# Optimization experiments

Hardware: AMD Instinct MI355X
Metric: run time of the kernel (lower is better)

The kernel has to match this reference:

```python
import jax, jax.numpy as jnp
import numpy as np
import math

D_MODEL = 1024
N_HEADS = 16
B, T = 4, 2048


def setup_inputs() -> dict:
    key = jax.random.key(0)
    ks = jax.random.split(key, 10)
    s = 1.0 / math.sqrt(D_MODEL)
    x = jax.random.normal(ks[0], (B, T, D_MODEL), dtype=jnp.float32)
    # causal mask, broadcastable over batch and heads; 0 -> masked
    mask = jnp.tril(jnp.ones((T, T), dtype=jnp.int32))[None, None, :, :]
    w_q = jax.random.normal(ks[1], (D_MODEL, D_MODEL), dtype=jnp.float32) * s
    b_q = jnp.zeros((D_MODEL,), dtype=jnp.float32)
    w_k = jax.random.normal(ks[2], (D_MODEL, D_MODEL), dtype=jnp.float32) * s
    b_k = jnp.zeros((D_MODEL,), dtype=jnp.float32)
    w_v = jax.random.normal(ks[3], (D_MODEL, D_MODEL), dtype=jnp.float32) * s
    b_v = jnp.zeros((D_MODEL,), dtype=jnp.float32)
    w_o = jax.random.normal(ks[4], (D_MODEL, D_MODEL), dtype=jnp.float32) * s
    b_o = jnp.zeros((D_MODEL,), dtype=jnp.float32)
    return {"x": x, "mask": mask, "w_q": w_q, "b_q": b_q, "w_k": w_k,
            "b_k": b_k, "w_v": w_v, "b_v": b_v, "w_o": w_o, "b_o": b_o}


def reference(x, mask, w_q, b_q, w_k, b_k, w_v, b_v, w_o, b_o):
    Bx, Tx, C = x.shape
    H = N_HEADS
    d_k = C // H
    def split_heads(y):  # [B,T,C] -> [B,H,T,d_k]
        return y.reshape(Bx, Tx, H, d_k).transpose(0, 2, 1, 3)
    Q = split_heads(x @ w_q + b_q)
    K = split_heads(x @ w_k + b_k)
    V = split_heads(x @ w_v + b_v)
    scores = jnp.einsum('bhqd,bhkd->bhqk', Q, K) / math.sqrt(d_k)
    scores = jnp.where(mask == 0, jnp.float32(-1e9), scores)
    attn = jax.nn.softmax(scores, axis=-1)
    out = jnp.einsum('bhqk,bhkd->bhqd', attn, V)
    out = out.transpose(0, 2, 1, 3).reshape(Bx, Tx, C)
    return out @ w_o + b_o
```

## Files before the change

### kernel.cpp

```cpp
#include <hip/hip_runtime.h>
#include <stdint.h>

#define D_MODEL 1024
#define NH      16
#define BB      4
#define TT      2048
#define MROWS   (BB * TT)

typedef __attribute__((ext_vector_type(8))) short bf16x8;
typedef __attribute__((ext_vector_type(4))) float f32x4;

__device__ __forceinline__ unsigned short f2bf(float f) {
    union { float f; unsigned int u; } v; v.f = f;
    unsigned int r = v.u + 0x7fffu + ((v.u >> 16) & 1u);
    return (unsigned short)(r >> 16);
}

__device__ __forceinline__ unsigned short f2bf_fast(float f) {
    union { float f; unsigned int u; } v; v.f = f;
    return (unsigned short)((v.u + 0x8000u) >> 16);
}

__device__ __forceinline__ void gload_lds16(const unsigned short* g, unsigned short* l) {
    __builtin_amdgcn_global_load_lds(
        (const __attribute__((address_space(1))) void*)g,
        (__attribute__((address_space(3))) void*)l,
        16, 0, 0);
}

__global__ void convert_x_kernel(const float* __restrict__ x, unsigned short* __restrict__ xb) {
    int i = blockIdx.x * 256 + threadIdx.x;
    float4 v = ((const float4*)x)[i];
    ushort4 o;
    o.x = f2bf(v.x); o.y = f2bf(v.y); o.z = f2bf(v.z); o.w = f2bf(v.w);
    ((ushort4*)xb)[i] = o;
}

__global__ void transpose_w_kernel(const float* __restrict__ wq, const float* __restrict__ wk,
                                   const float* __restrict__ wv, const float* __restrict__ wo,
                                   unsigned short* tq, unsigned short* tk,
                                   unsigned short* tv, unsigned short* to_) {
    const float* src; unsigned short* dst;
    switch (blockIdx.z) {
        case 0:  src = wq; dst = tq; break;
        case 1:  src = wk; dst = tk; break;
        case 2:  src = wv; dst = tv; break;
        default: src = wo; dst = to_; break;
    }
    __shared__ float tile[32][33];
    int tx = threadIdx.x & 31, ty = threadIdx.x >> 5;
    int k0 = blockIdx.y * 32, n0 = blockIdx.x * 32;
    #pragma unroll
    for (int i = 0; i < 4; ++i)
        tile[ty + i * 8][tx] = src[(k0 + ty + i * 8) * D_MODEL + n0 + tx];
    __syncthreads();
    #pragma unroll
    for (int i = 0; i < 4; ++i)
        dst[(n0 + ty + i * 8) * D_MODEL + k0 + tx] = f2bf(tile[tx][ty + i * 8]);
}

__device__ __forceinline__ void gemm_mainloop(const unsigned short* __restrict__ A,
                                              const unsigned short* __restrict__ Bt,
                                              int m0, int n0,
                                              unsigned short* As, unsigned short* Bs,
                                              f32x4 acc[4][4]) {
    const int tid = threadIdx.x;
    const int lane = tid & 63, wave = tid >> 6;
    const int wm = (wave >> 1) * 64, wn = (wave & 1) * 64;
    const int l15 = lane & 15, quad = lane >> 4;
    const int rx7 = l15 & 7;
    const int srow = tid >> 3;
    const int scol = ((tid & 7) ^ (srow & 7)) * 8;
    const unsigned short* Ag = A + (size_t)(m0 + srow) * D_MODEL + scol;
    const unsigned short* Bg = Bt + (size_t)(n0 + srow) * D_MODEL + scol;
    unsigned short* AsW = As + wave * 512;
    unsigned short* BsW = Bs + wave * 512;
    for (int k0 = 0; k0 < D_MODEL; k0 += 64) {
        __syncthreads();
        #pragma unroll
        for (int p = 0; p < 4; ++p) {
            gload_lds16(Ag + k0 + (size_t)(32 * p) * D_MODEL, AsW + (32 * p) * 64);
            gload_lds16(Bg + k0 + (size_t)(32 * p) * D_MODEL, BsW + (32 * p) * 64);
        }
        __syncthreads();
        #pragma unroll
        for (int kk = 0; kk < 2; ++kk) {
            const int co = ((kk * 4 + quad) ^ rx7) * 8;
            bf16x8 af[4], bfr[4];
            #pragma unroll
            for (int mt = 0; mt < 4; ++mt)
                af[mt] = *(const bf16x8*)(As + (wm + mt * 16 + l15) * 64 + co);
            #pragma unroll
            for (int nt = 0; nt < 4; ++nt)
                bfr[nt] = *(const bf16x8*)(Bs + (wn + nt * 16 + l15) * 64 + co);
            #pragma unroll
            for (int mt = 0; mt < 4; ++mt)
                #pragma unroll
                for (int nt = 0; nt < 4; ++nt)
                    acc[mt][nt] = __builtin_amdgcn_mfma_f32_16x16x32_bf16(af[mt], bfr[nt], acc[mt][nt], 0, 0, 0);
        }
    }
}

__global__ __launch_bounds__(256, 2) void gemm_qkv_kernel(
        const unsigned short* __restrict__ Xb, const unsigned short* __restrict__ Wt,
        const float* __restrict__ bq, const float* __restrict__ bk, const float* __restrict__ bv,
        unsigned short* __restrict__ Qo, unsigned short* __restrict__ Ko,
        unsigned short* __restrict__ VTo) {
    __shared__ unsigned short S[18432];
    unsigned short* As = S;
    unsigned short* Bs = S + 8192;
    int m0 = blockIdx.y * 128, n0 = blockIdx.x * 128;
    f32x4 acc[4][4];
    #pragma unroll
    for (int mt = 0; mt < 4; ++mt)
        #pragma unroll
        for (int nt = 0; nt < 4; ++nt)
            acc[mt][nt] = (f32x4){0.f, 0.f, 0.f, 0.f};
    gemm_mainloop(Xb, Wt, m0, n0, As, Bs, acc);

    const int sel = n0 >> 10;
    const float* bias = (sel == 0) ? bq : (sel == 1) ? bk : bv;
    const float scale = (sel == 0) ? 0.125f * 1.44269504f : 1.f;
    const int tid = threadIdx.x, lane = tid & 63, wave = tid >> 6;
    const int wm = (wave >> 1) * 64, wn = (wave & 1) * 64, l15 = lane & 15, quad = lane >> 4;
    if (sel < 2) {
        unsigned short* Out = (sel == 0) ? Qo : Ko;
        __syncthreads();
        unsigned short* R = S + (wn >> 6) * 9216;
        #pragma unroll
        for (int nt = 0; nt < 4; ++nt) {
            int ln = nt * 16 + l15;
            int col = (n0 + wn + nt * 16 + l15) & 1023;
            float bv_ = bias[col];
            #pragma unroll
            for (int mt = 0; mt < 4; ++mt)
                #pragma unroll
                for (int r = 0; r < 4; ++r) {
                    int lm = wm + mt * 16 + quad * 4 + r;
                    R[lm * 72 + ln] = f2bf((acc[mt][nt][r] + bv_) * scale);
                }
        }
        __syncthreads();
        int hh = tid >> 7, t = tid & 127;
        int h0 = (n0 & 1023) >> 6;
        int b = m0 >> 11, tb = m0 & 2047;
        unsigned short* gp = Out + (size_t)((b * NH + h0 + hh) * TT + tb + t) * 64;
        const unsigned short* lp = S + hh * 9216 + t * 72;
        #pragma unroll
        for (int j = 0; j < 8; ++j)
            *(uint4*)(gp + j * 8) = *(const uint4*)(lp + j * 8);
    } else {
        #pragma unroll
        for (int nt = 0; nt < 4; ++nt) {
            int col = (n0 + wn + nt * 16 + l15) & 1023;
            float bv_ = bias[col];
            int h = col >> 6, dd = col & 63;
            #pragma unroll
            for (int mt = 0; mt < 4; ++mt) {
                int gm0 = m0 + wm + mt * 16 + quad * 4;
                int b = gm0 >> 11, t0 = gm0 & 2047;
                ushort4 o;
                o.x = f2bf(acc[mt][nt][0] + bv_);
                o.y = f2bf(acc[mt][nt][1] + bv_);
                o.z = f2bf(acc[mt][nt][2] + bv_);
                o.w = f2bf(acc[mt][nt][3] + bv_);
                *(ushort4*)&VTo[(((size_t)(b * NH + h) * 16 + (t0 >> 7)) * 64 + dd) * 128 + (t0 & 127)] = o;
            }
        }
    }
}

__global__ __launch_bounds__(256, 2) void gemm_out_kernel(
        const unsigned short* __restrict__ Ob, const unsigned short* __restrict__ Wto,
        const float* __restrict__ bo, float* __restrict__ out) {
    __shared__ unsigned short As[128 * 64], Bs[128 * 64];
    int m0 = blockIdx.y * 128, n0 = blockIdx.x * 128;
    f32x4 acc[4][4];
    #pragma unroll
    for (int mt = 0; mt < 4; ++mt)
        #pragma unroll
        for (int nt = 0; nt < 4; ++nt)
            acc[mt][nt] = (f32x4){0.f, 0.f, 0.f, 0.f};
    gemm_mainloop(Ob, Wto, m0, n0, As, Bs, acc);
    const int tid = threadIdx.x, lane = tid & 63, wave = tid >> 6;
    const int wm = (wave >> 1) * 64, wn = (wave & 1) * 64, l15 = lane & 15, quad = lane >> 4;
    #pragma unroll
    for (int nt = 0; nt < 4; ++nt) {
        int gn = n0 + wn + nt * 16 + l15;
        float bv_ = bo[gn];
        #pragma unroll
        for (int mt = 0; mt < 4; ++mt) {
            #pragma unroll
            for (int r = 0; r < 4; ++r) {
                int gm = m0 + wm + mt * 16 + quad * 4 + r;
                out[(size_t)gm * D_MODEL + gn] = acc[mt][nt][r] + bv_;
            }
        }
    }
}

__global__ __launch_bounds__(256, 2) void flash_kernel(
        const unsigned short* __restrict__ Q, const unsigned short* __restrict__ K,
        const unsigned short* __restrict__ VT, unsigned short* __restrict__ O) {
    __shared__ unsigned short Kd[2][8192];
    __shared__ unsigned short Vd[2][8192];
    __shared__ unsigned short Ps[5120];
    const int n = blockIdx.x;
    const int bh = n & 63;
    const int qt = 15 - (n >> 6);
    const int q0 = qt * 128;
    const int tid = threadIdx.x, lane = tid & 63, wave = tid >> 6;
    const int l15 = lane & 15, quad = lane >> 4;
    const int mbase = wave * 32;
    const unsigned short* Qb = Q + (size_t)bh * (TT * 64) + (size_t)q0 * 64;
    const unsigned short* Kb = K + (size_t)bh * (TT * 64);
    const unsigned short* Vtb = VT + (size_t)bh * (16 * 8192);
    unsigned short* Pw = Ps + wave * 1280;

    int koff[4], voff[4];
    #pragma unroll
    for (int p = 0; p < 4; ++p) {
        int c = p * 256 + wave * 64 + lane;
        int kr = c >> 3, ks = c & 7;
        koff[p] = kr * 64 + ((ks ^ (kr & 7)) * 8);
        int vd = c >> 4, vs = c & 15;
        voff[p] = vd * 128 + ((vs ^ (vd & 15)) * 8);
    }
    auto fire = [&](int kt, int buf) {
        const unsigned short* Ksrc = Kb + kt * 8192;
        const unsigned short* Vsrc = Vtb + kt * 8192;
        #pragma unroll
        for (int p = 0; p < 4; ++p) {
            gload_lds16(Ksrc + koff[p], &Kd[buf][(p * 256 + wave * 64) * 8]);
            gload_lds16(Vsrc + voff[p], &Vd[buf][(p * 256 + wave * 64) * 8]);
        }
    };

    bf16x8 qf[2][2];
    #pragma unroll
    for (int mt = 0; mt < 2; ++mt)
        #pragma unroll
        for (int kk = 0; kk < 2; ++kk)
            qf[mt][kk] = *(const bf16x8*)(Qb + (size_t)(mbase + mt * 16 + l15) * 64 + kk * 32 + quad * 8);

    float l_part[2][4];
    f32x4 acc[2][4];
    #pragma unroll
    for (int mt = 0; mt < 2; ++mt) {
        #pragma unroll
        for (int r = 0; r < 4; ++r) l_part[mt][r] = 0.f;
        #pragma unroll
        for (int nt = 0; nt < 4; ++nt) acc[mt][nt] = (f32x4){0.f, 0.f, 0.f, 0.f};
    }

    fire(0, 0);

    for (int kt = 0; kt <= qt; ++kt) {
        const int p = kt & 1;
        __syncthreads();
        if (kt < qt) fire(kt + 1, p ^ 1);
        const unsigned short* Ksl = Kd[p];
        const unsigned short* Vsl = Vd[p];

        #pragma unroll 1
        for (int s4 = 0; s4 < 4; ++s4) {
            f32x4 sf[2][2];
            #pragma unroll
            for (int mt = 0; mt < 2; ++mt)
                #pragma unroll
                for (int ntl = 0; ntl < 2; ++ntl) sf[mt][ntl] = (f32x4){0.f, 0.f, 0.f, 0.f};
            #pragma unroll
            for (int kk = 0; kk < 2; ++kk)
                #pragma unroll
                for (int ntl = 0; ntl < 2; ++ntl) {
                    int row = s4 * 32 + ntl * 16 + l15;
                    bf16x8 kf = *(const bf16x8*)&Ksl[row * 64 + (((kk * 4 + quad) ^ (row & 7)) * 8)];
                    #pragma unroll
                    for (int mt = 0; mt < 2; ++mt)
                        sf[mt][ntl] = __builtin_amdgcn_mfma_f32_16x16x32_bf16(qf[mt][kk], kf, sf[mt][ntl], 0, 0, 0);
                }
            if (kt == qt) {
                #pragma unroll
                for (int mt = 0; mt < 2; ++mt)
                    #pragma unroll
                    for (int ntl = 0; ntl < 2; ++ntl)
                        #pragma unroll
                        for (int r = 0; r < 4; ++r) {
                            int qi = mbase + mt * 16 + quad * 4 + r;
                            int ki = s4 * 32 + ntl * 16 + l15;
                            if (ki > qi) sf[mt][ntl][r] = -1e30f;
                        }
            }
            #pragma unroll
            for (int mt = 0; mt < 2; ++mt)
                #pragma unroll
                for (int ntl = 0; ntl < 2; ++ntl)
                    #pragma unroll
                    for (int r = 0; r < 4; ++r) {
                        float pv = __builtin_amdgcn_exp2f(sf[mt][ntl][r]);
                        l_part[mt][r] += pv;
                        Pw[(mt * 16 + quad * 4 + r) * 40 + ntl * 16 + l15] = f2bf_fast(pv);
                    }
            bf16x8 pa[2];
            #pragma unroll
            for (int mt = 0; mt < 2; ++mt)
                pa[mt] = *(const bf16x8*)&Pw[(mt * 16 + l15) * 40 + quad * 8];
            #pragma unroll
            for (int ntv = 0; ntv < 4; ++ntv) {
                int d = ntv * 16 + l15;
                bf16x8 vf = *(const bf16x8*)&Vsl[d * 128 + (((s4 * 4 + quad) ^ (d & 15)) * 8)];
                #pragma unroll
                for (int mt = 0; mt < 2; ++mt)
                    acc[mt][ntv] = __builtin_amdgcn_mfma_f32_16x16x32_bf16(pa[mt], vf, acc[mt][ntv], 0, 0, 0);
            }
        }
    }

    const int b = bh >> 4, h = bh & 15;
    float inv[2][4];
    #pragma unroll
    for (int mt = 0; mt < 2; ++mt)
        #pragma unroll
        for (int r = 0; r < 4; ++r) {
            float l = l_part[mt][r];
            l += __shfl_xor(l, 1); l += __shfl_xor(l, 2);
            l += __shfl_xor(l, 4); l += __shfl_xor(l, 8);
            inv[mt][r] = __builtin_amdgcn_rcpf(l);
        }
    __syncthreads();
    unsigned short* Ost = &Kd[0][0];
    #pragma unroll
    for (int mt = 0; mt < 2; ++mt)
        #pragma unroll
        for (int nt = 0; nt < 4; ++nt)
            #pragma unroll
            for (int r = 0; r < 4; ++r)
                Ost[(mbase + mt * 16 + quad * 4 + r) * 72 + nt * 16 + l15] =
                    f2bf(acc[mt][nt][r] * inv[mt][r]);
    __syncthreads();
    {
        int row = tid >> 1, seg = tid & 1;
        unsigned short* gp = O + (size_t)(b * TT + q0 + row) * D_MODEL + h * 64 + seg * 32;
        const unsigned short* lp = Ost + row * 72 + seg * 32;
        #pragma unroll
        for (int j = 0; j < 4; ++j)
            *(uint4*)(gp + j * 8) = *(const uint4*)(lp + j * 8);
    }
}

extern "C" void kernel_launch(void* const* d_in, const int* in_sizes, int n_in,
                              void* d_out, int out_size, void* d_ws, size_t ws_size,
                              hipStream_t stream) {
    const float* x  = (const float*)d_in[0];
    const float* wq = (const float*)d_in[2];
    const float* bq = (const float*)d_in[3];
    const float* wk = (const float*)d_in[4];
    const float* bk = (const float*)d_in[5];
    const float* wv = (const float*)d_in[6];
    const float* bv = (const float*)d_in[7];
    const float* wo = (const float*)d_in[8];
    const float* bo = (const float*)d_in[9];

    char* ws = (char*)d_ws;
    unsigned short* Xb  = (unsigned short*)ws;
    unsigned short* Wtq = (unsigned short*)(ws + (size_t)(16 << 20));
    unsigned short* Wtk = Wtq + (size_t)D_MODEL * D_MODEL;
    unsigned short* Wtv = Wtk + (size_t)D_MODEL * D_MODEL;
    unsigned short* Wto = Wtv + (size_t)D_MODEL * D_MODEL;
    unsigned short* Qb  = Wto + (size_t)D_MODEL * D_MODEL;
    unsigned short* Kb  = Qb + (size_t)MROWS * D_MODEL;
    unsigned short* VTb = Kb + (size_t)MROWS * D_MODEL;
    unsigned short* Ob  = Xb;

    convert_x_kernel<<<(MROWS * D_MODEL) / (256 * 4), 256, 0, stream>>>(x, Xb);
    transpose_w_kernel<<<dim3(32, 32, 4), 256, 0, stream>>>(wq, wk, wv, wo, Wtq, Wtk, Wtv, Wto);
    gemm_qkv_kernel<<<dim3(3 * D_MODEL / 128, MROWS / 128), 256, 0, stream>>>(
        Xb, Wtq, bq, bk, bv, Qb, Kb, VTb);
    flash_kernel<<<dim3(16 * 64), 256, 0, stream>>>(Qb, Kb, VTb, Ob);
    gemm_out_kernel<<<dim3(D_MODEL / 128, MROWS / 128), 256, 0, stream>>>(Ob, Wto, bo, (float*)d_out);
}
```

Before: 252.3 us.

## Widen GEMM tiles to 128x256 and keep flash P in registers via transposed scores

The QKV and output GEMMs move from 128x128 to 128x256 tiles, with each wave computing 64x128, to raise arithmetic intensity and halve A-tile reloads. The QKV epilogue now stages Q/K heads through LDS in two phases. In the flash kernel the score MFMA operands are swapped so S comes out transposed, which lets the exp'd probabilities be packed straight into registers as bf16x4 and fed to a 16x16x16 MFMA against V. This removes the per-wave LDS round trip for P and shrinks the row-sum reduction. The cost is doubled accumulator registers in the GEMMs, which may hurt occupancy, and more, smaller K=16 MFMAs in the PV product.

```diff
diff --git a/kernel.cpp b/kernel.cpp
--- a/kernel.cpp
+++ b/kernel.cpp
@@ -8,7 +8,23 @@
 #define MROWS   (BB * TT)
 
 typedef __attribute__((ext_vector_type(8))) short bf16x8;
+typedef __attribute__((ext_vector_type(4))) short bf16x4;
 typedef __attribute__((ext_vector_type(4))) float f32x4;
+
+#if defined(__has_builtin)
+#if __has_builtin(__builtin_amdgcn_mfma_f32_16x16x16bf16_1k)
+#define MFMA16(a, b, c) __builtin_amdgcn_mfma_f32_16x16x16bf16_1k(a, b, c, 0, 0, 0)
+#elif __has_builtin(__builtin_amdgcn_mfma_f32_16x16x16_bf16_1k)
+#define MFMA16(a, b, c) __builtin_amdgcn_mfma_f32_16x16x16_bf16_1k(a, b, c, 0, 0, 0)
+#endif
+#endif
+#ifndef MFMA16
+static __device__ __forceinline__ f32x4 mfma16_asm(bf16x4 a, bf16x4 b, f32x4 c) {
+    asm volatile("v_mfma_f32_16x16x16_bf16 %0, %1, %2, %0" : "+v"(c) : "v"(a), "v"(b));
+    return c;
+}
+#define MFMA16(a, b, c) mfma16_asm(a, b, c)
+#endif
 
 __device__ __forceinline__ unsigned short f2bf(float f) {
     union { float f; unsigned int u; } v; v.f = f;
@@ -16,9 +32,9 @@
     return (unsigned short)(r >> 16);
 }
 
-__device__ __forceinline__ unsigned short f2bf_fast(float f) {
+__device__ __forceinline__ unsigned int f2bf_fast(float f) {
     union { float f; unsigned int u; } v; v.f = f;
-    return (unsigned short)((v.u + 0x8000u) >> 16);
+    return (v.u + 0x8000u) >> 16;
 }
 
 __device__ __forceinline__ void gload_lds16(const unsigned short* g, unsigned short* l) {
@@ -59,14 +75,14 @@
         dst[(n0 + ty + i * 8) * D_MODEL + k0 + tx] = f2bf(tile[tx][ty + i * 8]);
 }
 
-__device__ __forceinline__ void gemm_mainloop(const unsigned short* __restrict__ A,
-                                              const unsigned short* __restrict__ Bt,
-                                              int m0, int n0,
-                                              unsigned short* As, unsigned short* Bs,
-                                              f32x4 acc[4][4]) {
+__device__ __forceinline__ void gemm_mainloop256(const unsigned short* __restrict__ A,
+                                                 const unsigned short* __restrict__ Bt,
+                                                 int m0, int n0,
+                                                 unsigned short* As, unsigned short* Bs,
+                                                 f32x4 acc[4][8]) {
     const int tid = threadIdx.x;
     const int lane = tid & 63, wave = tid >> 6;
-    const int wm = (wave >> 1) * 64, wn = (wave & 1) * 64;
+    const int wm = (wave >> 1) * 64, wn = (wave & 1) * 128;
     const int l15 = lane & 15, quad = lane >> 4;
     const int rx7 = l15 & 7;
     const int srow = tid >> 3;
@@ -78,25 +94,26 @@
     for (int k0 = 0; k0 < D_MODEL; k0 += 64) {
         __syncthreads();
         #pragma unroll
-        for (int p = 0; p < 4; ++p) {
+        for (int p = 0; p < 4; ++p)
             gload_lds16(Ag + k0 + (size_t)(32 * p) * D_MODEL, AsW + (32 * p) * 64);
+        #pragma unroll
+        for (int p = 0; p < 8; ++p)
             gload_lds16(Bg + k0 + (size_t)(32 * p) * D_MODEL, BsW + (32 * p) * 64);
-        }
         __syncthreads();
         #pragma unroll
         for (int kk = 0; kk < 2; ++kk) {
             const int co = ((kk * 4 + quad) ^ rx7) * 8;
-            bf16x8 af[4], bfr[4];
+            bf16x8 af[4], bfr[8];
             #pragma unroll
             for (int mt = 0; mt < 4; ++mt)
                 af[mt] = *(const bf16x8*)(As + (wm + mt * 16 + l15) * 64 + co);
             #pragma unroll
-            for (int nt = 0; nt < 4; ++nt)
+            for (int nt = 0; nt < 8; ++nt)
                 bfr[nt] = *(const bf16x8*)(Bs + (wn + nt * 16 + l15) * 64 + co);
             #pragma unroll
             for (int mt = 0; mt < 4; ++mt)
                 #pragma unroll
-                for (int nt = 0; nt < 4; ++nt)
+                for (int nt = 0; nt < 8; ++nt)
                     acc[mt][nt] = __builtin_amdgcn_mfma_f32_16x16x32_bf16(af[mt], bfr[nt], acc[mt][nt], 0, 0, 0);
         }
     }
@@ -107,52 +124,59 @@
         const float* __restrict__ bq, const float* __restrict__ bk, const float* __restrict__ bv,
         unsigned short* __restrict__ Qo, unsigned short* __restrict__ Ko,
         unsigned short* __restrict__ VTo) {
-    __shared__ unsigned short S[18432];
+    __shared__ unsigned short S[24576];
     unsigned short* As = S;
     unsigned short* Bs = S + 8192;
-    int m0 = blockIdx.y * 128, n0 = blockIdx.x * 128;
-    f32x4 acc[4][4];
+    int m0 = blockIdx.y * 128, n0 = blockIdx.x * 256;
+    f32x4 acc[4][8];
     #pragma unroll
     for (int mt = 0; mt < 4; ++mt)
         #pragma unroll
-        for (int nt = 0; nt < 4; ++nt)
+        for (int nt = 0; nt < 8; ++nt)
             acc[mt][nt] = (f32x4){0.f, 0.f, 0.f, 0.f};
-    gemm_mainloop(Xb, Wt, m0, n0, As, Bs, acc);
+    gemm_mainloop256(Xb, Wt, m0, n0, As, Bs, acc);
 
     const int sel = n0 >> 10;
     const float* bias = (sel == 0) ? bq : (sel == 1) ? bk : bv;
     const float scale = (sel == 0) ? 0.125f * 1.44269504f : 1.f;
     const int tid = threadIdx.x, lane = tid & 63, wave = tid >> 6;
-    const int wm = (wave >> 1) * 64, wn = (wave & 1) * 64, l15 = lane & 15, quad = lane >> 4;
+    const int wm = (wave >> 1) * 64, wn = (wave & 1) * 128, l15 = lane & 15, quad = lane >> 4;
     if (sel < 2) {
         unsigned short* Out = (sel == 0) ? Qo : Ko;
+        const int h0 = (n0 & 1023) >> 6;
+        const int b = m0 >> 11, tb = m0 & 2047;
+        unsigned short* R = S + (wn >> 7) * 9216;
         __syncthreads();
-        unsigned short* R = S + (wn >> 6) * 9216;
-        #pragma unroll
-        for (int nt = 0; nt < 4; ++nt) {
-            int ln = nt * 16 + l15;
-            int col = (n0 + wn + nt * 16 + l15) & 1023;
-            float bv_ = bias[col];
-            #pragma unroll
-            for (int mt = 0; mt < 4; ++mt)
-                #pragma unroll
-                for (int r = 0; r < 4; ++r) {
-                    int lm = wm + mt * 16 + quad * 4 + r;
-                    R[lm * 72 + ln] = f2bf((acc[mt][nt][r] + bv_) * scale);
-                }
-        }
-        __syncthreads();
-        int hh = tid >> 7, t = tid & 127;
-        int h0 = (n0 & 1023) >> 6;
-        int b = m0 >> 11, tb = m0 & 2047;
-        unsigned short* gp = Out + (size_t)((b * NH + h0 + hh) * TT + tb + t) * 64;
-        const unsigned short* lp = S + hh * 9216 + t * 72;
-        #pragma unroll
-        for (int j = 0; j < 8; ++j)
-            *(uint4*)(gp + j * 8) = *(const uint4*)(lp + j * 8);
+        #pragma unroll
+        for (int ph = 0; ph < 2; ++ph) {
+            #pragma unroll
+            for (int nt = ph * 4; nt < ph * 4 + 4; ++nt) {
+                int col = n0 + wn + nt * 16 + l15;
+                float bv_ = bias[col & 1023];
+                int ln = (nt & 3) * 16 + l15;
+                #pragma unroll
+                for (int mt = 0; mt < 4; ++mt)
+                    #pragma unroll
+                    for (int r = 0; r < 4; ++r) {
+                        int lm = wm + mt * 16 + quad * 4 + r;
+                        R[lm * 72 + ln] = f2bf((acc[mt][nt][r] + bv_) * scale);
+                    }
+            }
+            __syncthreads();
+            {
+                int hsel = tid >> 7, t = tid & 127;
+                int head = h0 + ph + hsel * 2;
+                unsigned short* gp = Out + (size_t)((b * NH + head) * TT + tb + t) * 64;
+                const unsigned short* lp = S + hsel * 9216 + t * 72;
+                #pragma unroll
+                for (int j = 0; j < 8; ++j)
+                    *(uint4*)(gp + j * 8) = *(const uint4*)(lp + j * 8);
+            }
+            if (ph == 0) __syncthreads();
+        }
     } else {
         #pragma unroll
-        for (int nt = 0; nt < 4; ++nt) {
+        for (int nt = 0; nt < 8; ++nt) {
             int col = (n0 + wn + nt * 16 + l15) & 1023;
             float bv_ = bias[col];
             int h = col >> 6, dd = col & 63;
@@ -174,19 +198,19 @@
 __global__ __launch_bounds__(256, 2) void gemm_out_kernel(
         const unsigned short* __restrict__ Ob, const unsigned short* __restrict__ Wto,
         const float* __restrict__ bo, float* __restrict__ out) {
-    __shared__ unsigned short As[128 * 64], Bs[128 * 64];
-    int m0 = blockIdx.y * 128, n0 = blockIdx.x * 128;
-    f32x4 acc[4][4];
+    __shared__ unsigned short As[8192], Bs[16384];
+    int m0 = blockIdx.y * 128, n0 = blockIdx.x * 256;
+    f32x4 acc[4][8];
     #pragma unroll
     for (int mt = 0; mt < 4; ++mt)
         #pragma unroll
-        for (int nt = 0; nt < 4; ++nt)
+        for (int nt = 0; nt < 8; ++nt)
             acc[mt][nt] = (f32x4){0.f, 0.f, 0.f, 0.f};
-    gemm_mainloop(Ob, Wto, m0, n0, As, Bs, acc);
+    gemm_mainloop256(Ob, Wto, m0, n0, As, Bs, acc);
     const int tid = threadIdx.x, lane = tid & 63, wave = tid >> 6;
-    const int wm = (wave >> 1) * 64, wn = (wave & 1) * 64, l15 = lane & 15, quad = lane >> 4;
-    #pragma unroll
-    for (int nt = 0; nt < 4; ++nt) {
+    const int wm = (wave >> 1) * 64, wn = (wave & 1) * 128, l15 = lane & 15, quad = lane >> 4;
+    #pragma unroll
+    for (int nt = 0; nt < 8; ++nt) {
         int gn = n0 + wn + nt * 16 + l15;
         float bv_ = bo[gn];
         #pragma unroll
@@ -205,7 +229,6 @@
         const unsigned short* __restrict__ VT, unsigned short* __restrict__ O) {
     __shared__ unsigned short Kd[2][8192];
     __shared__ unsigned short Vd[2][8192];
-    __shared__ unsigned short Ps[5120];
     const int n = blockIdx.x;
     const int bh = n & 63;
     const int qt = 15 - (n >> 6);
@@ -216,7 +239,6 @@
     const unsigned short* Qb = Q + (size_t)bh * (TT * 64) + (size_t)q0 * 64;
     const unsigned short* Kb = K + (size_t)bh * (TT * 64);
     const unsigned short* Vtb = VT + (size_t)bh * (16 * 8192);
-    unsigned short* Pw = Ps + wave * 1280;
 
     int koff[4], voff[4];
     #pragma unroll
@@ -244,15 +266,12 @@
         for (int kk = 0; kk < 2; ++kk)
             qf[mt][kk] = *(const bf16x8*)(Qb + (size_t)(mbase + mt * 16 + l15) * 64 + kk * 32 + quad * 8);
 
-    float l_part[2][4];
+    float l_part[2] = {0.f, 0.f};
     f32x4 acc[2][4];
     #pragma unroll
-    for (int mt = 0; mt < 2; ++mt) {
-        #pragma unroll
-        for (int r = 0; r < 4; ++r) l_part[mt][r] = 0.f;
+    for (int mt = 0; mt < 2; ++mt)
         #pragma unroll
         for (int nt = 0; nt < 4; ++nt) acc[mt][nt] = (f32x4){0.f, 0.f, 0.f, 0.f};
-    }
 
     fire(0, 0);
 
@@ -264,80 +283,87 @@
         const unsigned short* Vsl = Vd[p];
 
         #pragma unroll 1
-        for (int s4 = 0; s4 < 4; ++s4) {
-            f32x4 sf[2][2];
+        for (int s2 = 0; s2 < 2; ++s2) {
+            f32x4 sf[2][4];
             #pragma unroll
             for (int mt = 0; mt < 2; ++mt)
                 #pragma unroll
-                for (int ntl = 0; ntl < 2; ++ntl) sf[mt][ntl] = (f32x4){0.f, 0.f, 0.f, 0.f};
+                for (int k4 = 0; k4 < 4; ++k4) sf[mt][k4] = (f32x4){0.f, 0.f, 0.f, 0.f};
             #pragma unroll
             for (int kk = 0; kk < 2; ++kk)
                 #pragma unroll
-                for (int ntl = 0; ntl < 2; ++ntl) {
-                    int row = s4 * 32 + ntl * 16 + l15;
+                for (int k4 = 0; k4 < 4; ++k4) {
+                    int row = s2 * 64 + k4 * 16 + l15;
                     bf16x8 kf = *(const bf16x8*)&Ksl[row * 64 + (((kk * 4 + quad) ^ (row & 7)) * 8)];
                     #pragma unroll
                     for (int mt = 0; mt < 2; ++mt)
-                        sf[mt][ntl] = __builtin_amdgcn_mfma_f32_16x16x32_bf16(qf[mt][kk], kf, sf[mt][ntl], 0, 0, 0);
+                        sf[mt][k4] = __builtin_amdgcn_mfma_f32_16x16x32_bf16(kf, qf[mt][kk], sf[mt][k4], 0, 0, 0);
                 }
             if (kt == qt) {
                 #pragma unroll
                 for (int mt = 0; mt < 2; ++mt)
                     #pragma unroll
-                    for (int ntl = 0; ntl < 2; ++ntl)
+                    for (int k4 = 0; k4 < 4; ++k4)
                         #pragma unroll
                         for (int r = 0; r < 4; ++r) {
-                            int qi = mbase + mt * 16 + quad * 4 + r;
-                            int ki = s4 * 32 + ntl * 16 + l15;
-                            if (ki > qi) sf[mt][ntl][r] = -1e30f;
+                            int qi = mbase + mt * 16 + l15;
+                            int ki = s2 * 64 + k4 * 16 + quad * 4 + r;
+                            if (ki > qi) sf[mt][k4][r] = -1e30f;
                         }
             }
+            bf16x4 pf[2][4];
             #pragma unroll
             for (int mt = 0; mt < 2; ++mt)
                 #pragma unroll
-                for (int ntl = 0; ntl < 2; ++ntl)
+                for (int k4 = 0; k4 < 4; ++k4) {
+                    float e0 = __builtin_amdgcn_exp2f(sf[mt][k4][0]);
+                    float e1 = __builtin_amdgcn_exp2f(sf[mt][k4][1]);
+                    float e2 = __builtin_amdgcn_exp2f(sf[mt][k4][2]);
+                    float e3 = __builtin_amdgcn_exp2f(sf[mt][k4][3]);
+                    l_part[mt] += (e0 + e1) + (e2 + e3);
+                    union { unsigned int u[2]; bf16x4 v; } pk;
+                    pk.u[0] = (f2bf_fast(e1) << 16) | f2bf_fast(e0);
+                    pk.u[1] = (f2bf_fast(e3) << 16) | f2bf_fast(e2);
+                    pf[mt][k4] = pk.v;
+                }
+            #pragma unroll
+            for (int k4 = 0; k4 < 4; ++k4) {
+                int kb = s2 * 64 + k4 * 16 + quad * 4;
+                int chunk = kb >> 3, within = kb & 7;
+                #pragma unroll
+                for (int ntv = 0; ntv < 4; ++ntv) {
+                    int d = ntv * 16 + l15;
+                    bf16x4 va = *(const bf16x4*)&Vsl[d * 128 + ((chunk ^ (d & 15)) * 8) + within];
                     #pragma unroll
-                    for (int r = 0; r < 4; ++r) {
-                        float pv = __builtin_amdgcn_exp2f(sf[mt][ntl][r]);
-                        l_part[mt][r] += pv;
-                        Pw[(mt * 16 + quad * 4 + r) * 40 + ntl * 16 + l15] = f2bf_fast(pv);
-                    }
-            bf16x8 pa[2];
-            #pragma unroll
-            for (int mt = 0; mt < 2; ++mt)
-                pa[mt] = *(const bf16x8*)&Pw[(mt * 16 + l15) * 40 + quad * 8];
-            #pragma unroll
-            for (int ntv = 0; ntv < 4; ++ntv) {
-                int d = ntv * 16 + l15;
-                bf16x8 vf = *(const bf16x8*)&Vsl[d * 128 + (((s4 * 4 + quad) ^ (d & 15)) * 8)];
-                #pragma unroll
-                for (int mt = 0; mt < 2; ++mt)
-                    acc[mt][ntv] = __builtin_amdgcn_mfma_f32_16x16x32_bf16(pa[mt], vf, acc[mt][ntv], 0, 0, 0);
+                    for (int mt = 0; mt < 2; ++mt)
+                        acc[mt][ntv] = MFMA16(va, pf[mt][k4], acc[mt][ntv]);
+                }
             }
         }
     }
 
     const int b = bh >> 4, h = bh & 15;
-    float inv[2][4];
-    #pragma unroll
-    for (int mt = 0; mt < 2; ++mt)
-        #pragma unroll
-        for (int r = 0; r < 4; ++r) {
-            float l = l_part[mt][r];
-            l += __shfl_xor(l, 1); l += __shfl_xor(l, 2);
-            l += __shfl_xor(l, 4); l += __shfl_xor(l, 8);
-            inv[mt][r] = __builtin_amdgcn_rcpf(l);
-        }
+    float inv[2];
+    #pragma unroll
+    for (int mt = 0; mt < 2; ++mt) {
+        float l = l_part[mt];
+        l += __shfl_xor(l, 16);
+        l += __shfl_xor(l, 32);
+        inv[mt] = __builtin_amdgcn_rcpf(l);
+    }
     __syncthreads();
     unsigned short* Ost = &Kd[0][0];
     #pragma unroll
     for (int mt = 0; mt < 2; ++mt)
         #pragma unroll
-        for (int nt = 0; nt < 4; ++nt)
-            #pragma unroll
-            for (int r = 0; r < 4; ++r)
-                Ost[(mbase + mt * 16 + quad * 4 + r) * 72 + nt * 16 + l15] =
-                    f2bf(acc[mt][nt][r] * inv[mt][r]);
+        for (int ntv = 0; ntv < 4; ++ntv) {
+            ushort4 o;
+            o.x = f2bf(acc[mt][ntv][0] * inv[mt]);
+            o.y = f2bf(acc[mt][ntv][1] * inv[mt]);
+            o.z = f2bf(acc[mt][ntv][2] * inv[mt]);
+            o.w = f2bf(acc[mt][ntv][3] * inv[mt]);
+            *(ushort4*)&Ost[(mbase + mt * 16 + l15) * 72 + ntv * 16 + quad * 4] = o;
+        }
     __syncthreads();
     {
         int row = tid >> 1, seg = tid & 1;
@@ -375,8 +401,8 @@
 
     convert_x_kernel<<<(MROWS * D_MODEL) / (256 * 4), 256, 0, stream>>>(x, Xb);
     transpose_w_kernel<<<dim3(32, 32, 4), 256, 0, stream>>>(wq, wk, wv, wo, Wtq, Wtk, Wtv, Wto);
-    gemm_qkv_kernel<<<dim3(3 * D_MODEL / 128, MROWS / 128), 256, 0, stream>>>(
+    gemm_qkv_kernel<<<dim3(3 * D_MODEL / 256, MROWS / 128), 256, 0, stream>>>(
         Xb, Wtq, bq, bk, bv, Qb, Kb, VTb);
     flash_kernel<<<dim3(16 * 64), 256, 0, stream>>>(Qb, Kb, VTb, Ob);
-    gemm_out_kernel<<<dim3(D_MODEL / 128, MROWS / 128), 256, 0, stream>>>(Ob, Wto, bo, (float*)d_out);
-}
+    gemm_out_kernel<<<dim3(D_MODEL / 256, MROWS / 128), 256, 0, stream>>>(Ob, Wto, bo, (float*)d_out);
+}
```

Measured after the change: 267.3 us. 1.06x slower.
